# Kernel optimization log

Hardware: AMD Instinct MI355X
Metric: run time of the kernel (lower is better)

The kernel has to match this reference:

```python
import jax, jax.numpy as jnp
import numpy as np

C = 16; HP = 16; WP = 16; D = 32; KITER = 4; P = 8; N = P * P; B = 16; HID = 64


def conv2d(x, w, b):
    # x: (B, Cin, H, W), w: (Cout, Cin, kh, kw), 'same' padding for 3x3
    y = jax.lax.conv_general_dilated(x, w, (1, 1), [(1, 1), (1, 1)],
                                     dimension_numbers=('NCHW', 'OIHW', 'NCHW'))
    return y + b[None, :, None, None]


def setup_inputs() -> dict:
    key = jax.random.key(0)
    ks = jax.random.split(key, 20)
    n = lambda k, shape, s=0.1: jax.random.normal(k, shape, jnp.float32) * s
    # 4-neighbor directed grid edges over P x P nodes
    edges = []
    for p in range(P):
        for q in range(P):
            i = p * P + q
            for dp, dq in ((0, 1), (1, 0), (0, -1), (-1, 0)):
                pp, qq = p + dp, q + dq
                if 0 <= pp < P and 0 <= qq < P:
                    edges.append((i, pp * P + qq))
    edge_index = jnp.asarray(np.asarray(edges, np.int32))  # (E, 2) with (i=dst, j=src)
    return {
        'seed': n(ks[0], (B, C, P * HP, P * WP), 1.0),
        'edge_index': edge_index,
        'wq': n(ks[1], (C, D)), 'bq': jnp.zeros((D,), jnp.float32),
        'wk': n(ks[2], (C, D)), 'bk': jnp.zeros((D,), jnp.float32),
        'wm': n(ks[3], (C, C, 3, 3)), 'bm': jnp.zeros((C,), jnp.float32),
        'a_w1': n(ks[4], (2 * D, HID)), 'a_b1': jnp.zeros((HID,), jnp.float32),
        'a_w2': n(ks[5], (HID, HID)), 'a_b2': jnp.zeros((HID,), jnp.float32),
        'a_wo': n(ks[6], (HID, 1)), 'a_bo': jnp.zeros((1,), jnp.float32),
        'g_w': n(ks[7], (C, 1, 3, 3)), 'g_b': jnp.zeros((C,), jnp.float32),
        'gru_wg': n(ks[8], (2 * C, 2 * C, 3, 3)), 'gru_bg': jnp.zeros((2 * C,), jnp.float32),
        'gru_wc': n(ks[9], (C, 2 * C, 3, 3)), 'gru_bc': jnp.zeros((C,), jnp.float32),
    }


def reference(seed, edge_index, wq, bq, wk, bk, wm, bm,
              a_w1, a_b1, a_w2, a_b2, a_wo, a_bo,
              g_w, g_b, gru_wg, gru_bg, gru_wc, gru_bc):
    Bb, Cc, PH, PW = seed.shape
    Pp = PH // HP
    Nn = Pp * Pp
    # patchify: (B,C,PH,PW) -> (B,N,C,H,W), node order is row-major (p,q)
    X = seed.reshape(Bb, Cc, Pp, HP, Pp, WP).transpose(0, 2, 4, 1, 3, 5).reshape(Bb, Nn, Cc, HP, WP)
    ei = edge_index[:, 0]  # dst node i
    ej = edge_index[:, 1]  # src node j
    # GateConv on a spatially-constant map e: conv(e*ones) = e * conv(ones) (+bias).
    ones_map = jnp.ones((1, 1, HP, WP), seed.dtype)
    T = jax.lax.conv_general_dilated(ones_map, g_w, (1, 1), [(1, 1), (1, 1)],
                                     dimension_numbers=('NCHW', 'OIHW', 'NCHW'))  # (1,C,H,W)
    for _ in range(KITER):
        xm = X.mean((-2, -1))  # (B,N,C); mean commutes with the 1x1 convs f_Q/f_K
        q_vec = xm @ wq + bq   # (B,N,d)
        k_vec = xm @ wk + bk
        M = conv2d(X.reshape(Bb * Nn, Cc, HP, WP), wm, bm).reshape(Bb, Nn, Cc, HP, WP)
        # per-edge attention scores via ConcatMLP
        h0 = jnp.concatenate([q_vec[:, ei], k_vec[:, ej]], axis=-1)  # (B,E,2d)
        h1 = jax.nn.relu(h0 @ a_w1 + a_b1)
        h2 = jax.nn.relu(h1 @ a_w2 + a_b2)
        e = (h2 @ a_wo + a_bo)[..., 0]  # (B,E)
        # gate map and gated messages
        G = jax.nn.sigmoid(e[:, :, None, None, None] * T[None] + g_b[None, None, :, None, None])  # (B,E,C,H,W)
        msg = G * M[:, ej]  # gather src patches, gate
        agg = jax.ops.segment_sum(jnp.moveaxis(msg, 1, 0), ei, num_segments=Nn)  # (N,B,C,H,W)
        M_agg = jnp.moveaxis(agg, 0, 1).reshape(Bb * Nn, Cc, HP, WP)
        # ConvGRU cell update
        h = X.reshape(Bb * Nn, Cc, HP, WP)
        zr = jax.nn.sigmoid(conv2d(jnp.concatenate([M_agg, h], axis=1), gru_wg, gru_bg))
        z, r = zr[:, :Cc], zr[:, Cc:]
        cand = jnp.tanh(conv2d(jnp.concatenate([M_agg, r * h], axis=1), gru_wc, gru_bc))
        X = ((1.0 - z) * h + z * cand).reshape(Bb, Nn, Cc, HP, WP)
    # unpatchify
    out = X.reshape(Bb, Pp, Pp, Cc, HP, WP).transpose(0, 3, 1, 4, 2, 5).reshape(Bb, Cc, PH, PW)
    return out
```

## Files before the change

### kernel.cpp

```cpp
#include <hip/hip_runtime.h>
#include <hip/hip_bf16.h>
#include <hip/hip_cooperative_groups.h>

namespace cg = cooperative_groups;

#define Bt 16
#define Ct 16
#define Nt 64
#define KITERt 4

#define WF_TOTAL 25681
#define SWZ_TOTAL 16384
#define SETUP_IDX (WF_TOTAL + 4096 + Nt + SWZ_TOTAL)
#define SAH_STRIDE 40

typedef __attribute__((ext_vector_type(8))) short bf16x8;
typedef __attribute__((ext_vector_type(4))) short s16x4;
typedef __attribute__((ext_vector_type(4))) float f32x4;

__device__ inline short f2bs(float f) {
    __hip_bfloat16 h = __float2bfloat16(f);
    short s; __builtin_memcpy(&s, &h, 2); return s;
}
__device__ inline float bs2f(short s) {
    __hip_bfloat16 h; __builtin_memcpy(&h, &s, 2);
    return __bfloat162float(h);
}
__device__ inline float loadf(const void* p, int i, int isf32) {
    return isf32 ? ((const float*)p)[i]
                 : __bfloat162float(((const __hip_bfloat16*)p)[i]);
}
__device__ inline float sigm(float x) {
    return __builtin_amdgcn_rcpf(1.f + __expf(-x));
}
__device__ inline float tanh_fast(float x) {
    float e = __expf(2.f * x);
    return 1.f - 2.f * __builtin_amdgcn_rcpf(e + 1.f);
}

__global__ __launch_bounds__(256)
__attribute__((amdgpu_waves_per_eu(4, 4)))
void fused_kernel(
    const void* __restrict__ seed,
    const void* __restrict__ wq, const void* __restrict__ bq,
    const void* __restrict__ wk, const void* __restrict__ bk,
    const void* __restrict__ wm, const void* __restrict__ bm,
    const void* __restrict__ w1, const void* __restrict__ b1,
    const void* __restrict__ w2, const void* __restrict__ b2,
    const void* __restrict__ wo, const void* __restrict__ bo,
    const void* __restrict__ gw, const void* __restrict__ gb,
    const void* __restrict__ wg, const void* __restrict__ bg,
    const void* __restrict__ wc, const void* __restrict__ bc,
    const int* __restrict__ edge, int E,
    float* __restrict__ Wf, float* __restrict__ Tpix,
    int* __restrict__ counts, int* __restrict__ nbrs,
    __hip_bfloat16* __restrict__ swz,
    float* __restrict__ qv0, float* __restrict__ kv0,
    float* __restrict__ qv1, float* __restrict__ kv1,
    float* __restrict__ Mb0, float* __restrict__ Mb1,
    void* __restrict__ out)
{
    __shared__ float sred[4];
    __shared__ int sflag;
    __shared__ float xred[64];
    __shared__ int snb[256];
    __shared__ float evs[4];
    __shared__ __align__(16) short sAH[324 * SAH_STRIDE];
    int bn = blockIdx.x, t = threadIdx.x;
    int b = bn >> 6, i = bn & 63;
    int lane = t & 63, wv = t >> 6;
    int quad = lane >> 4, n16 = lane & 15;
    int pp = ((t >> 4) + 1) * 18 + (t & 15) + 1;

    const short* WgSg = (const short*)swz;
    const short* WcSg = (const short*)(swz + 9216);
    const short* WmSg = (const short*)(swz + 13824);

    {
        float v = fabsf(__bfloat162float(((const __hip_bfloat16*)seed)[t]));
        if (!(v <= 1e30f)) v = 1e30f;
#pragma unroll
        for (int off = 1; off < 64; off <<= 1) v = fmaxf(v, __shfl_xor(v, off, 64));
        if (lane == 0) sred[wv] = v;
        __syncthreads();
        if (t == 0) {
            float m = fmaxf(fmaxf(sred[0], sred[1]), fmaxf(sred[2], sred[3]));
            sflag = (m > 1e10f) ? 1 : 0;
        }
        __syncthreads();
    }
    int isf32 = sflag;

    if (bn == 0) {
        snb[t] = 0;
        __syncthreads();
        for (int e = t; e < E; e += 256) {
            int ei = edge[2 * e], ej = edge[2 * e + 1];
            int d = ej - ei;
            int slot = (d == 1) ? 0 : (d == 8) ? 1 : (d == -1) ? 2 : 3;
            snb[ei * 4 + slot] = ej + 1;
        }
        __syncthreads();
        if (t < 64) {
            int dcount = 0;
            int outv[4] = {0, 0, 0, 0};
#pragma unroll
            for (int s = 0; s < 4; ++s) {
                int v = snb[t * 4 + s];
                if (v) outv[dcount++] = v - 1;
            }
            counts[t] = dcount;
#pragma unroll
            for (int s = 0; s < 4; ++s) nbrs[t * 4 + s] = outv[s];
        }
    }

    int idx = bn * 256 + t;
    if (idx < WF_TOTAL) {
        int ii = idx;
        const void* base;
        if (ii < 512) base = wq;
        else if ((ii -= 512) < 32) base = bq;
        else if ((ii -= 32) < 512) base = wk;
        else if ((ii -= 512) < 32) base = bk;
        else if ((ii -= 32) < 2304) base = wm;
        else if ((ii -= 2304) < 16) base = bm;
        else if ((ii -= 16) < 4096) base = w1;
        else if ((ii -= 4096) < 64) base = b1;
        else if ((ii -= 64) < 4096) base = w2;
        else if ((ii -= 4096) < 64) base = b2;
        else if ((ii -= 64) < 64) base = wo;
        else if ((ii -= 64) < 1) base = bo;
        else if ((ii -= 1) < 16) base = gb;
        else if ((ii -= 16) < 9216) base = wg;
        else if ((ii -= 9216) < 32) base = bg;
        else if ((ii -= 32) < 4608) base = wc;
        else { ii -= 4608; base = bc; }
        Wf[idx] = loadf(base, ii, isf32);
    } else if (idx < WF_TOTAL + 4096) {
        int j = idx - WF_TOTAL;
        int pix = j >> 4, ch = j & 15;
        int y = pix >> 4, x = pix & 15;
        float s = 0.f;
        for (int ky = 0; ky < 3; ++ky)
            for (int kx = 0; kx < 3; ++kx) {
                int yy = y + ky - 1, xx = x + kx - 1;
                if (yy >= 0 && yy < 16 && xx >= 0 && xx < 16)
                    s += loadf(gw, ch * 9 + ky * 3 + kx, isf32);
            }
        Tpix[j] = s;
    } else if (idx >= WF_TOTAL + 4096 + Nt && idx < SETUP_IDX) {
        int j = idx - (WF_TOTAL + 4096 + Nt);
        float val;
        if (j < 9216) {
            int sn = j >> 9, rem = j & 511;
            int ln = rem >> 3, jj = rem & 7;
            int s = sn >> 1, nt = sn & 1;
            int ci = (ln >> 4) * 8 + jj;
            int co = nt * 16 + (ln & 15);
            val = loadf(wg, co * 288 + ci * 9 + s, isf32);
        } else if (j < 9216 + 4608) {
            int j1 = j - 9216;
            int s = j1 >> 9, rem = j1 & 511;
            int ln = rem >> 3, jj = rem & 7;
            int ci = (ln >> 4) * 8 + jj;
            int co = ln & 15;
            val = loadf(wc, co * 288 + ci * 9 + s, isf32);
        } else {
            int j2 = j - 13824;
            int sp = j2 >> 9, rem = j2 & 511;
            int ln = rem >> 3, jj = rem & 7;
            int k = (ln >> 4) * 8 + jj;
            int s = sp * 2 + (k >> 4);
            int ci = k & 15;
            int co = ln & 15;
            val = (s <= 8) ? loadf(wm, co * 144 + ci * 9 + s, isf32) : 0.f;
        }
        swz[j] = __float2bfloat16(val);
    }

    {
        int n = bn & 63;
        int pq = n >> 3, qq = n & 7;
        int y = t >> 4, x = t & 15;
        float v[16];
#pragma unroll
        for (int c = 0; c < 16; ++c)
            v[c] = loadf(seed, ((b * 16 + c) * 128 + pq * 16 + y) * 128 + qq * 16 + x, isf32);
        bf16x8 o0, o1;
#pragma unroll
        for (int c = 0; c < 8; ++c) { o0[c] = f2bs(v[c]); o1[c] = f2bs(v[8 + c]); }

        for (int p = t; p < 324; p += 256) {
            int yy = p / 18 - 1, xx = p % 18 - 1;
            if (!((unsigned)yy < 16u && (unsigned)xx < 16u)) {
                bf16x8 z = {0, 0, 0, 0, 0, 0, 0, 0};
                short* row = sAH + p * SAH_STRIDE;
                *(bf16x8*)(row) = z;      *(bf16x8*)(row + 8) = z;
                *(bf16x8*)(row + 16) = z; *(bf16x8*)(row + 24) = z;
            }
        }
        {
            short* row = sAH + pp * SAH_STRIDE;
            *(bf16x8*)(row) = o0;      *(bf16x8*)(row + 8) = o1;
            *(bf16x8*)(row + 16) = o0; *(bf16x8*)(row + 24) = o1;
        }

#pragma unroll
        for (int c = 0; c < 16; ++c) {
            float s = v[c];
#pragma unroll
            for (int off = 1; off < 64; off <<= 1) s += __shfl_xor(s, off, 64);
            if (lane == c) xred[wv * 16 + c] = s;
        }
        __syncthreads();
        if (t < 64) {
            int d = t & 31;
            float a = (t < 32) ? loadf(bq, d, isf32) : loadf(bk, d, isf32);
#pragma unroll
            for (int c = 0; c < 16; ++c) {
                float xm = (xred[c] + xred[16 + c] + xred[32 + c] + xred[48 + c]) * (1.f / 256.f);
                a += xm * ((t < 32) ? loadf(wq, c * 32 + d, isf32)
                                    : loadf(wk, c * 32 + d, isf32));
            }
            if (t < 32) qv0[bn * 32 + d] = a; else kv0[bn * 32 + d] = a;
        }

        float bm_l = loadf(bm, n16, isf32);
        f32x4 accM[4];
#pragma unroll
        for (int mt = 0; mt < 4; ++mt) accM[mt] = (f32x4){bm_l, bm_l, bm_l, bm_l};
#pragma unroll
        for (int sp = 0; sp < 5; ++sp) {
            int s2 = sp * 2 + (quad >> 1);
            int valid = (s2 <= 8);
            int s2c = valid ? s2 : 8;
            int ky = s2c / 3, kx = s2c - ky * 3;
            bf16x8 Bf;
#pragma unroll
            for (int j = 0; j < 8; ++j) {
                short bv = 0;
                if (valid) bv = f2bs(loadf(wm, n16 * 144 + ((quad & 1) * 8 + j) * 9 + s2, isf32));
                Bf[j] = bv;
            }
            int cib = (quad & 1) * 8;
#pragma unroll
            for (int mt = 0; mt < 4; ++mt) {
                int pc = (wv * 4 + mt + ky) * 18 + n16 + kx;
                bf16x8 A = *(const bf16x8*)(sAH + pc * SAH_STRIDE + cib);
                accM[mt] = __builtin_amdgcn_mfma_f32_16x16x32_bf16(A, Bf, accM[mt], 0, 0, 0);
            }
        }
        float* mo = Mb0 + bn * 4096;
#pragma unroll
        for (int mt = 0; mt < 4; ++mt)
#pragma unroll
            for (int r = 0; r < 4; ++r) {
                int pix = (wv * 4 + mt) * 16 + quad * 4 + r;
                mo[pix * 16 + n16] = accM[mt][r];
            }
    }

    __threadfence();
    cg::this_grid().sync();

    int4 nb4 = *(const int4*)(nbrs + i * 4);
    int deg = counts[i];
    int ejl[4] = {nb4.x, nb4.y, nb4.z, nb4.w};

    for (int it = 0; it < KITERt; ++it) {
        const float* Min  = (it & 1) ? Mb1 : Mb0;
        float*       Mout = (it & 1) ? Mb0 : Mb1;
        const float* qin  = (it & 1) ? qv1 : qv0;
        const float* kin  = (it & 1) ? kv1 : kv0;
        float*       qout = (it & 1) ? qv0 : qv1;
        float*       kout = (it & 1) ? kv0 : kv1;
        int last = (it == KITERt - 1);

        if (wv < deg) {
            int ej = ejl[wv];
            float h0 = (lane < 32) ? qin[bn * 32 + lane]
                                   : kin[(b * 64 + ej) * 32 + (lane - 32)];
            const float* W1 = Wf + 3408;
            const float* W2 = Wf + 7568;
            float p0 = 0.f, p1 = 0.f, p2 = 0.f, p3 = 0.f;
#pragma unroll
            for (int j = 0; j < 64; j += 4) {
                p0 += __shfl(h0, j + 0, 64) * W1[(j + 0) * 64 + lane];
                p1 += __shfl(h0, j + 1, 64) * W1[(j + 1) * 64 + lane];
                p2 += __shfl(h0, j + 2, 64) * W1[(j + 2) * 64 + lane];
                p3 += __shfl(h0, j + 3, 64) * W1[(j + 3) * 64 + lane];
            }
            float a1 = fmaxf(Wf[7504 + lane] + ((p0 + p1) + (p2 + p3)), 0.f);
            p0 = p1 = p2 = p3 = 0.f;
#pragma unroll
            for (int j = 0; j < 64; j += 4) {
                p0 += __shfl(a1, j + 0, 64) * W2[(j + 0) * 64 + lane];
                p1 += __shfl(a1, j + 1, 64) * W2[(j + 1) * 64 + lane];
                p2 += __shfl(a1, j + 2, 64) * W2[(j + 2) * 64 + lane];
                p3 += __shfl(a1, j + 3, 64) * W2[(j + 3) * 64 + lane];
            }
            float a2 = fmaxf(Wf[11664 + lane] + ((p0 + p1) + (p2 + p3)), 0.f);
            float pe = a2 * Wf[11728 + lane];
#pragma unroll
            for (int off = 32; off; off >>= 1) pe += __shfl_down(pe, off, 64);
            if (lane == 0) evs[wv] = pe + Wf[11792];
        }
        __syncthreads();

        float magg[16];
#pragma unroll
        for (int c = 0; c < 16; ++c) magg[c] = 0.f;
        {
            float Tp[16];
#pragma unroll
            for (int c = 0; c < 4; ++c)
                *(f32x4*)(Tp + 4 * c) = *(const f32x4*)(Tpix + t * 16 + 4 * c);
#pragma unroll
            for (int ii = 0; ii < 4; ++ii)
                if (ii < deg) {
                    const float* mp = Min + (b * 64 + ejl[ii]) * 4096 + t * 16;
                    f32x4 m0 = *(const f32x4*)(mp);
                    f32x4 m1 = *(const f32x4*)(mp + 4);
                    f32x4 m2 = *(const f32x4*)(mp + 8);
                    f32x4 m3 = *(const f32x4*)(mp + 12);
                    float evv = evs[ii];
#pragma unroll
                    for (int c = 0; c < 4; ++c) {
                        magg[c]      += sigm(evv * Tp[c]      + Wf[11793 + c])      * m0[c];
                        magg[c + 4]  += sigm(evv * Tp[c + 4]  + Wf[11793 + c + 4])  * m1[c];
                        magg[c + 8]  += sigm(evv * Tp[c + 8]  + Wf[11793 + c + 8])  * m2[c];
                        magg[c + 12] += sigm(evv * Tp[c + 12] + Wf[11793 + c + 12]) * m3[c];
                    }
                }
        }
        {
            bf16x8 mg0, mg1;
#pragma unroll
            for (int c = 0; c < 8; ++c) { mg0[c] = f2bs(magg[c]); mg1[c] = f2bs(magg[c + 8]); }
            *(bf16x8*)(sAH + pp * SAH_STRIDE) = mg0;
            *(bf16x8*)(sAH + pp * SAH_STRIDE + 8) = mg1;
        }
        __syncthreads();

        float bz = Wf[21025 + n16], br = Wf[21025 + 16 + n16];
        f32x4 accZ[4], accR[4];
#pragma unroll
        for (int mt = 0; mt < 4; ++mt) {
            accZ[mt] = (f32x4){bz, bz, bz, bz};
            accR[mt] = (f32x4){br, br, br, br};
        }
#pragma unroll
        for (int s = 0; s < 9; ++s) {
            int ky = s / 3, kx = s - (s / 3) * 3;
            bf16x8 B0 = *(const bf16x8*)(WgSg + (s * 2 + 0) * 512 + lane * 8);
            bf16x8 B1 = *(const bf16x8*)(WgSg + (s * 2 + 1) * 512 + lane * 8);
#pragma unroll
            for (int mt = 0; mt < 4; ++mt) {
                int pc = (wv * 4 + mt + ky) * 18 + n16 + kx;
                bf16x8 A = *(const bf16x8*)(sAH + pc * SAH_STRIDE + quad * 8);
                accZ[mt] = __builtin_amdgcn_mfma_f32_16x16x32_bf16(A, B0, accZ[mt], 0, 0, 0);
                accR[mt] = __builtin_amdgcn_mfma_f32_16x16x32_bf16(A, B1, accR[mt], 0, 0, 0);
            }
        }
        float zf[16], hf[16], rh[16];
#pragma unroll
        for (int mt = 0; mt < 4; ++mt)
#pragma unroll
            for (int r = 0; r < 4; ++r) {
                int k = mt * 4 + r;
                int ps = (wv * 4 + mt + 1) * 18 + quad * 4 + r + 1;
                hf[k] = bs2f(sAH[ps * SAH_STRIDE + 16 + n16]);
                zf[k] = sigm(accZ[mt][r]);
                rh[k] = sigm(accR[mt][r]) * hf[k];
            }
        __syncthreads();
#pragma unroll
        for (int mt = 0; mt < 4; ++mt)
#pragma unroll
            for (int r = 0; r < 4; ++r) {
                int ps = (wv * 4 + mt + 1) * 18 + quad * 4 + r + 1;
                sAH[ps * SAH_STRIDE + 16 + n16] = f2bs(rh[mt * 4 + r]);
            }
        __syncthreads();

        float bcl = Wf[25665 + n16];
        f32x4 accC[4];
#pragma unroll
        for (int mt = 0; mt < 4; ++mt) accC[mt] = (f32x4){bcl, bcl, bcl, bcl};
#pragma unroll
        for (int s = 0; s < 9; ++s) {
            int ky = s / 3, kx = s - (s / 3) * 3;
            bf16x8 Bc = *(const bf16x8*)(WcSg + s * 512 + lane * 8);
#pragma unroll
            for (int mt = 0; mt < 4; ++mt) {
                int pc = (wv * 4 + mt + ky) * 18 + n16 + kx;
                bf16x8 A = *(const bf16x8*)(sAH + pc * SAH_STRIDE + quad * 8);
                accC[mt] = __builtin_amdgcn_mfma_f32_16x16x32_bf16(A, Bc, accC[mt], 0, 0, 0);
            }
        }
        float nxv[16];
#pragma unroll
        for (int mt = 0; mt < 4; ++mt)
#pragma unroll
            for (int r = 0; r < 4; ++r) {
                int k = mt * 4 + r;
                nxv[k] = (1.f - zf[k]) * hf[k] + zf[k] * tanh_fast(accC[mt][r]);
            }

        if (last) {
            int pq = i >> 3, qq = i & 7;
#pragma unroll
            for (int mt = 0; mt < 4; ++mt) {
                long base = ((long)(b * 16 + n16) * 128 + pq * 16 + wv * 4 + mt) * 128
                            + qq * 16 + quad * 4;
                if (isf32) {
                    f32x4 v = {nxv[mt * 4], nxv[mt * 4 + 1], nxv[mt * 4 + 2], nxv[mt * 4 + 3]};
                    *(f32x4*)((float*)out + base) = v;
                } else {
                    s16x4 v = {f2bs(nxv[mt * 4]), f2bs(nxv[mt * 4 + 1]),
                               f2bs(nxv[mt * 4 + 2]), f2bs(nxv[mt * 4 + 3])};
                    *(s16x4*)((short*)out + base) = v;
                }
            }
            return;
        }

        __syncthreads();

        float ssum = 0.f;
#pragma unroll
        for (int mt = 0; mt < 4; ++mt)
#pragma unroll
            for (int r = 0; r < 4; ++r) {
                int k = mt * 4 + r;
                ssum += nxv[k];
                int p = (wv * 4 + mt + 1) * 18 + quad * 4 + r + 1;
                short vb = f2bs(nxv[k]);
                sAH[p * SAH_STRIDE + n16] = vb;
                sAH[p * SAH_STRIDE + 16 + n16] = vb;
            }
        ssum += __shfl_xor(ssum, 16, 64);
        ssum += __shfl_xor(ssum, 32, 64);
        if (lane < 16) xred[wv * 16 + lane] = ssum;
        __syncthreads();

        float bm_l = Wf[3392 + n16];
        f32x4 accM[4];
#pragma unroll
        for (int mt = 0; mt < 4; ++mt) accM[mt] = (f32x4){bm_l, bm_l, bm_l, bm_l};
#pragma unroll
        for (int sp = 0; sp < 5; ++sp) {
            bf16x8 Bf = *(const bf16x8*)(WmSg + sp * 512 + lane * 8);
            int s2 = sp * 2 + (quad >> 1);
            if (s2 > 8) s2 = 8;
            int ky = s2 / 3, kx = s2 - (s2 / 3) * 3;
            int cib = (quad & 1) * 8;
#pragma unroll
            for (int mt = 0; mt < 4; ++mt) {
                int pc = (wv * 4 + mt + ky) * 18 + n16 + kx;
                bf16x8 A = *(const bf16x8*)(sAH + pc * SAH_STRIDE + cib);
                accM[mt] = __builtin_amdgcn_mfma_f32_16x16x32_bf16(A, Bf, accM[mt], 0, 0, 0);
            }
        }
        {
            float* mo = Mout + bn * 4096;
#pragma unroll
            for (int mt = 0; mt < 4; ++mt)
#pragma unroll
                for (int r = 0; r < 4; ++r) {
                    int pix = (wv * 4 + mt) * 16 + quad * 4 + r;
                    mo[pix * 16 + n16] = accM[mt][r];
                }
        }
        if (t < 64) {
            int d = t & 31;
            const float* W = (t < 32) ? Wf : Wf + 544;
            float a = (t < 32) ? Wf[512 + d] : Wf[1056 + d];
#pragma unroll
            for (int c = 0; c < 16; ++c) {
                float xc = (xred[c] + xred[16 + c] + xred[32 + c] + xred[48 + c]) * (1.f / 256.f);
                a += xc * W[c * 32 + d];
            }
            if (t < 32) qout[bn * 32 + d] = a; else kout[bn * 32 + d] = a;
        }
        __threadfence();
        cg::this_grid().sync();
    }
}

__global__ __launch_bounds__(256) void setup_kernel(
    const void* __restrict__ seed,
    const void* __restrict__ wq, const void* __restrict__ bq,
    const void* __restrict__ wk, const void* __restrict__ bk,
    const void* __restrict__ wm, const void* __restrict__ bm,
    const void* __restrict__ w1, const void* __restrict__ b1,
    const void* __restrict__ w2, const void* __restrict__ b2,
    const void* __restrict__ wo, const void* __restrict__ bo,
    const void* __restrict__ gw, const void* __restrict__ gb,
    const void* __restrict__ wg, const void* __restrict__ bg,
    const void* __restrict__ wc, const void* __restrict__ bc,
    const int* __restrict__ edge, int E,
    float* __restrict__ Wf, float* __restrict__ Tpix,
// ... 187 lines not shown
                bf16x8 A = *(const bf16x8*)(sM + pc * SAH_STRIDE + cib);
                accM[mt] = __builtin_amdgcn_mfma_f32_16x16x32_bf16(A, Bf, accM[mt], 0, 0, 0);
            }
        }
        float* mo = M0 + bn * 4096;
#pragma unroll
        for (int mt = 0; mt < 4; ++mt)
#pragma unroll
            for (int r = 0; r < 4; ++r) {
                int pix = (wv * 4 + mt) * 16 + quad * 4 + r;
                mo[pix * 16 + n16] = accM[mt][r];
            }
    }
}

__global__ __launch_bounds__(256, 4) void iter_kernel(
    const short* __restrict__ Xin, short* __restrict__ Xout,
    const float* __restrict__ Min, float* __restrict__ Mout,
    const float* __restrict__ qin, const float* __restrict__ kin,
    float* __restrict__ qout, float* __restrict__ kout,
    const float* __restrict__ Tpix,
    const short* __restrict__ WmS,
    const short* __restrict__ WgS,
    const short* __restrict__ WcS,
    const float* __restrict__ Wf,
    const int* __restrict__ counts, const int* __restrict__ nbrs,
    const int* __restrict__ flagp, void* __restrict__ out, int last)
{
    __shared__ __align__(16) short sAH[324 * SAH_STRIDE];
    __shared__ float evs[4];
// ... 260 lines not shown
    __hip_bfloat16* swz = (__hip_bfloat16*)(ws + 4355600);
    float* Mb0 = ws + 4363792;
    float* Mb1 = ws + 8558096;

    const short* WgS = (const short*)swz;
    const short* WcS = (const short*)(swz + 9216);
    const short* WmS = (const short*)(swz + 13824);

    static int coop_ok = -1;
    if (coop_ok < 0) {
        int dev = 0, ncu = 0, coop = 0;
        hipFuncAttributes attr;
        hipError_t e1 = hipGetDevice(&dev);
        hipDeviceProp_t prop;
        hipError_t e2 = (e1 == hipSuccess) ? hipGetDeviceProperties(&prop, dev) : e1;
        hipError_t e3 = hipFuncGetAttributes(&attr, (const void*)fused_kernel);
        if (e2 == hipSuccess) { ncu = prop.multiProcessorCount; coop = prop.cooperativeLaunch; }
        coop_ok = (e2 == hipSuccess && e3 == hipSuccess && coop &&
                   attr.numRegs > 0 && attr.numRegs <= 128 &&
                   attr.localSizeBytes == 0 &&
                   (long)ncu * 4 >= (long)(Bt * Nt)) ? 1 : 0;
        (void)hipGetLastError();
    }

    if (coop_ok == 1) {
        const void* wq = d_in[2];  const void* bq = d_in[3];
        const void* wk = d_in[4];  const void* bk = d_in[5];
        const void* wm = d_in[6];  const void* bm = d_in[7];
        const void* w1 = d_in[8];  const void* b1 = d_in[9];
        const void* w2 = d_in[10]; const void* b2 = d_in[11];
        const void* wo = d_in[12]; const void* bo = d_in[13];
        const void* gw = d_in[14]; const void* gb = d_in[15];
        const void* wg = d_in[16]; const void* bg = d_in[17];
        const void* wc = d_in[18]; const void* bc = d_in[19];
        void* outp = d_out;

        void* kargs[] = {
            (void*)&seed,
            (void*)&wq, (void*)&bq, (void*)&wk, (void*)&bk,
            (void*)&wm, (void*)&bm, (void*)&w1, (void*)&b1,
            (void*)&w2, (void*)&b2, (void*)&wo, (void*)&bo,
            (void*)&gw, (void*)&gb, (void*)&wg, (void*)&bg,
            (void*)&wc, (void*)&bc,
            (void*)&edge, (void*)&E,
            (void*)&Wf, (void*)&Tpix, (void*)&counts, (void*)&nbrs,
            (void*)&swz,
            (void*)&qv0, (void*)&kv0, (void*)&qv1, (void*)&kv1,
            (void*)&Mb0, (void*)&Mb1, (void*)&outp
        };
        hipError_t rc = hipLaunchCooperativeKernel(
            (const void*)fused_kernel, dim3(Bt * Nt), dim3(256), kargs, 0, stream);
        if (rc == hipSuccess) return;
        (void)hipGetLastError();
        coop_ok = 0;
    }

    setup_kernel<<<Bt * Nt, 256, 0, stream>>>(
        seed,
        d_in[2], d_in[3], d_in[4], d_in[5], d_in[6], d_in[7], d_in[8], d_in[9],
        d_in[10], d_in[11], d_in[12], d_in[13], d_in[14], d_in[15], d_in[16],
        d_in[17], d_in[18], d_in[19],
        edge, E, Wf, Tpix, counts, nbrs, swz, Xb0, qv0, kv0, Mb0, flag);

    short* Xs[2] = {Xb0, Xb1};
    float* Ms[2] = {Mb0, Mb1};
    float* qs[2] = {qv0, qv1};
    float* ks[2] = {kv0, kv1};
    for (int it = 0; it < KITERt; ++it) {
        int in = it & 1, on = in ^ 1;
        int last = (it == KITERt - 1);
        iter_kernel<<<Bt * Nt, 256, 0, stream>>>(
            Xs[in], Xs[on], Ms[in], Ms[on], qs[in], ks[in], qs[on], ks[on],
            Tpix, WmS, WgS, WcS, Wf, counts, nbrs, flag, d_out, last);
    }
}
```

Before: 226.4 us.

## Split fused cooperative kernel into normal setup launch plus cooperative iteration kernel

Replaces the single cooperative kernel that did setup and all iterations with a regular setup_kernel launch followed by a cooperative iter4_kernel that runs the four GRU iterations with grid syncs between them. The setup phase no longer needs the grid-wide barrier and can run at its own occupancy. The iteration kernel reads pre-staged X from global memory instead of rebuilding it. This adds one extra kernel launch and a global round trip for the initial state in exchange for a lighter cooperative kernel.

```diff
diff --git a/kernel.cpp b/kernel.cpp
--- a/kernel.cpp
+++ b/kernel.cpp
@@ -36,457 +36,6 @@
 __device__ inline float tanh_fast(float x) {
     float e = __expf(2.f * x);
     return 1.f - 2.f * __builtin_amdgcn_rcpf(e + 1.f);
-}
-
-__global__ __launch_bounds__(256)
-__attribute__((amdgpu_waves_per_eu(4, 4)))
-void fused_kernel(
-    const void* __restrict__ seed,
-    const void* __restrict__ wq, const void* __restrict__ bq,
-    const void* __restrict__ wk, const void* __restrict__ bk,
-    const void* __restrict__ wm, const void* __restrict__ bm,
-    const void* __restrict__ w1, const void* __restrict__ b1,
-    const void* __restrict__ w2, const void* __restrict__ b2,
-    const void* __restrict__ wo, const void* __restrict__ bo,
-    const void* __restrict__ gw, const void* __restrict__ gb,
-    const void* __restrict__ wg, const void* __restrict__ bg,
-    const void* __restrict__ wc, const void* __restrict__ bc,
-    const int* __restrict__ edge, int E,
-    float* __restrict__ Wf, float* __restrict__ Tpix,
-    int* __restrict__ counts, int* __restrict__ nbrs,
-    __hip_bfloat16* __restrict__ swz,
-    float* __restrict__ qv0, float* __restrict__ kv0,
-    float* __restrict__ qv1, float* __restrict__ kv1,
-    float* __restrict__ Mb0, float* __restrict__ Mb1,
-    void* __restrict__ out)
-{
-    __shared__ float sred[4];
-    __shared__ int sflag;
-    __shared__ float xred[64];
-    __shared__ int snb[256];
-    __shared__ float evs[4];
-    __shared__ __align__(16) short sAH[324 * SAH_STRIDE];
-    int bn = blockIdx.x, t = threadIdx.x;
-    int b = bn >> 6, i = bn & 63;
-    int lane = t & 63, wv = t >> 6;
-    int quad = lane >> 4, n16 = lane & 15;
-    int pp = ((t >> 4) + 1) * 18 + (t & 15) + 1;
-
-    const short* WgSg = (const short*)swz;
-    const short* WcSg = (const short*)(swz + 9216);
-    const short* WmSg = (const short*)(swz + 13824);
-
-    {
-        float v = fabsf(__bfloat162float(((const __hip_bfloat16*)seed)[t]));
-        if (!(v <= 1e30f)) v = 1e30f;
-#pragma unroll
-        for (int off = 1; off < 64; off <<= 1) v = fmaxf(v, __shfl_xor(v, off, 64));
-        if (lane == 0) sred[wv] = v;
-        __syncthreads();
-        if (t == 0) {
-            float m = fmaxf(fmaxf(sred[0], sred[1]), fmaxf(sred[2], sred[3]));
-            sflag = (m > 1e10f) ? 1 : 0;
-        }
-        __syncthreads();
-    }
-    int isf32 = sflag;
-
-    if (bn == 0) {
-        snb[t] = 0;
-        __syncthreads();
-        for (int e = t; e < E; e += 256) {
-            int ei = edge[2 * e], ej = edge[2 * e + 1];
-            int d = ej - ei;
-            int slot = (d == 1) ? 0 : (d == 8) ? 1 : (d == -1) ? 2 : 3;
-            snb[ei * 4 + slot] = ej + 1;
-        }
-        __syncthreads();
-        if (t < 64) {
-            int dcount = 0;
-            int outv[4] = {0, 0, 0, 0};
-#pragma unroll
-            for (int s = 0; s < 4; ++s) {
-                int v = snb[t * 4 + s];
-                if (v) outv[dcount++] = v - 1;
-            }
-            counts[t] = dcount;
-#pragma unroll
-            for (int s = 0; s < 4; ++s) nbrs[t * 4 + s] = outv[s];
-        }
-    }
-
-    int idx = bn * 256 + t;
-    if (idx < WF_TOTAL) {
-        int ii = idx;
-        const void* base;
-        if (ii < 512) base = wq;
-        else if ((ii -= 512) < 32) base = bq;
-        else if ((ii -= 32) < 512) base = wk;
-        else if ((ii -= 512) < 32) base = bk;
-        else if ((ii -= 32) < 2304) base = wm;
-        else if ((ii -= 2304) < 16) base = bm;
-        else if ((ii -= 16) < 4096) base = w1;
-        else if ((ii -= 4096) < 64) base = b1;
-        else if ((ii -= 64) < 4096) base = w2;
-        else if ((ii -= 4096) < 64) base = b2;
-        else if ((ii -= 64) < 64) base = wo;
-        else if ((ii -= 64) < 1) base = bo;
-        else if ((ii -= 1) < 16) base = gb;
-        else if ((ii -= 16) < 9216) base = wg;
-        else if ((ii -= 9216) < 32) base = bg;
-        else if ((ii -= 32) < 4608) base = wc;
-        else { ii -= 4608; base = bc; }
-        Wf[idx] = loadf(base, ii, isf32);
-    } else if (idx < WF_TOTAL + 4096) {
-        int j = idx - WF_TOTAL;
-        int pix = j >> 4, ch = j & 15;
-        int y = pix >> 4, x = pix & 15;
-        float s = 0.f;
-        for (int ky = 0; ky < 3; ++ky)
-            for (int kx = 0; kx < 3; ++kx) {
-                int yy = y + ky - 1, xx = x + kx - 1;
-                if (yy >= 0 && yy < 16 && xx >= 0 && xx < 16)
-                    s += loadf(gw, ch * 9 + ky * 3 + kx, isf32);
-            }
-        Tpix[j] = s;
-    } else if (idx >= WF_TOTAL + 4096 + Nt && idx < SETUP_IDX) {
-        int j = idx - (WF_TOTAL + 4096 + Nt);
-        float val;
-        if (j < 9216) {
-            int sn = j >> 9, rem = j & 511;
-            int ln = rem >> 3, jj = rem & 7;
-            int s = sn >> 1, nt = sn & 1;
-            int ci = (ln >> 4) * 8 + jj;
-            int co = nt * 16 + (ln & 15);
-            val = loadf(wg, co * 288 + ci * 9 + s, isf32);
-        } else if (j < 9216 + 4608) {
-            int j1 = j - 9216;
-            int s = j1 >> 9, rem = j1 & 511;
-            int ln = rem >> 3, jj = rem & 7;
-            int ci = (ln >> 4) * 8 + jj;
-            int co = ln & 15;
-            val = loadf(wc, co * 288 + ci * 9 + s, isf32);
-        } else {
-            int j2 = j - 13824;
-            int sp = j2 >> 9, rem = j2 & 511;
-            int ln = rem >> 3, jj = rem & 7;
-            int k = (ln >> 4) * 8 + jj;
-            int s = sp * 2 + (k >> 4);
-            int ci = k & 15;
-            int co = ln & 15;
-            val = (s <= 8) ? loadf(wm, co * 144 + ci * 9 + s, isf32) : 0.f;
-        }
-        swz[j] = __float2bfloat16(val);
-    }
-
-    {
-        int n = bn & 63;
-        int pq = n >> 3, qq = n & 7;
-        int y = t >> 4, x = t & 15;
-        float v[16];
-#pragma unroll
-        for (int c = 0; c < 16; ++c)
-            v[c] = loadf(seed, ((b * 16 + c) * 128 + pq * 16 + y) * 128 + qq * 16 + x, isf32);
-        bf16x8 o0, o1;
-#pragma unroll
-        for (int c = 0; c < 8; ++c) { o0[c] = f2bs(v[c]); o1[c] = f2bs(v[8 + c]); }
-
-        for (int p = t; p < 324; p += 256) {
-            int yy = p / 18 - 1, xx = p % 18 - 1;
-            if (!((unsigned)yy < 16u && (unsigned)xx < 16u)) {
-                bf16x8 z = {0, 0, 0, 0, 0, 0, 0, 0};
-                short* row = sAH + p * SAH_STRIDE;
-                *(bf16x8*)(row) = z;      *(bf16x8*)(row + 8) = z;
-                *(bf16x8*)(row + 16) = z; *(bf16x8*)(row + 24) = z;
-            }
-        }
-        {
-            short* row = sAH + pp * SAH_STRIDE;
-            *(bf16x8*)(row) = o0;      *(bf16x8*)(row + 8) = o1;
-            *(bf16x8*)(row + 16) = o0; *(bf16x8*)(row + 24) = o1;
-        }
-
-#pragma unroll
-        for (int c = 0; c < 16; ++c) {
-            float s = v[c];
-#pragma unroll
-            for (int off = 1; off < 64; off <<= 1) s += __shfl_xor(s, off, 64);
-            if (lane == c) xred[wv * 16 + c] = s;
-        }
-        __syncthreads();
-        if (t < 64) {
-            int d = t & 31;
-            float a = (t < 32) ? loadf(bq, d, isf32) : loadf(bk, d, isf32);
-#pragma unroll
-            for (int c = 0; c < 16; ++c) {
-                float xm = (xred[c] + xred[16 + c] + xred[32 + c] + xred[48 + c]) * (1.f / 256.f);
-                a += xm * ((t < 32) ? loadf(wq, c * 32 + d, isf32)
-                                    : loadf(wk, c * 32 + d, isf32));
-            }
-            if (t < 32) qv0[bn * 32 + d] = a; else kv0[bn * 32 + d] = a;
-        }
-
-        float bm_l = loadf(bm, n16, isf32);
-        f32x4 accM[4];
-#pragma unroll
-        for (int mt = 0; mt < 4; ++mt) accM[mt] = (f32x4){bm_l, bm_l, bm_l, bm_l};
-#pragma unroll
-        for (int sp = 0; sp < 5; ++sp) {
-            int s2 = sp * 2 + (quad >> 1);
-            int valid = (s2 <= 8);
-            int s2c = valid ? s2 : 8;
-            int ky = s2c / 3, kx = s2c - ky * 3;
-            bf16x8 Bf;
-#pragma unroll
-            for (int j = 0; j < 8; ++j) {
-                short bv = 0;
-                if (valid) bv = f2bs(loadf(wm, n16 * 144 + ((quad & 1) * 8 + j) * 9 + s2, isf32));
-                Bf[j] = bv;
-            }
-            int cib = (quad & 1) * 8;
-#pragma unroll
-            for (int mt = 0; mt < 4; ++mt) {
-                int pc = (wv * 4 + mt + ky) * 18 + n16 + kx;
-                bf16x8 A = *(const bf16x8*)(sAH + pc * SAH_STRIDE + cib);
-                accM[mt] = __builtin_amdgcn_mfma_f32_16x16x32_bf16(A, Bf, accM[mt], 0, 0, 0);
-            }
-        }
-        float* mo = Mb0 + bn * 4096;
-#pragma unroll
-        for (int mt = 0; mt < 4; ++mt)
-#pragma unroll
-            for (int r = 0; r < 4; ++r) {
-                int pix = (wv * 4 + mt) * 16 + quad * 4 + r;
-                mo[pix * 16 + n16] = accM[mt][r];
-            }
-    }
-
-    __threadfence();
-    cg::this_grid().sync();
-
-    int4 nb4 = *(const int4*)(nbrs + i * 4);
-    int deg = counts[i];
-    int ejl[4] = {nb4.x, nb4.y, nb4.z, nb4.w};
-
-    for (int it = 0; it < KITERt; ++it) {
-        const float* Min  = (it & 1) ? Mb1 : Mb0;
-        float*       Mout = (it & 1) ? Mb0 : Mb1;
-        const float* qin  = (it & 1) ? qv1 : qv0;
-        const float* kin  = (it & 1) ? kv1 : kv0;
-        float*       qout = (it & 1) ? qv0 : qv1;
-        float*       kout = (it & 1) ? kv0 : kv1;
-        int last = (it == KITERt - 1);
-
-        if (wv < deg) {
-            int ej = ejl[wv];
-            float h0 = (lane < 32) ? qin[bn * 32 + lane]
-                                   : kin[(b * 64 + ej) * 32 + (lane - 32)];
-            const float* W1 = Wf + 3408;
-            const float* W2 = Wf + 7568;
-            float p0 = 0.f, p1 = 0.f, p2 = 0.f, p3 = 0.f;
-#pragma unroll
-            for (int j = 0; j < 64; j += 4) {
-                p0 += __shfl(h0, j + 0, 64) * W1[(j + 0) * 64 + lane];
-                p1 += __shfl(h0, j + 1, 64) * W1[(j + 1) * 64 + lane];
-                p2 += __shfl(h0, j + 2, 64) * W1[(j + 2) * 64 + lane];
-                p3 += __shfl(h0, j + 3, 64) * W1[(j + 3) * 64 + lane];
-            }
-            float a1 = fmaxf(Wf[7504 + lane] + ((p0 + p1) + (p2 + p3)), 0.f);
-            p0 = p1 = p2 = p3 = 0.f;
-#pragma unroll
-            for (int j = 0; j < 64; j += 4) {
-                p0 += __shfl(a1, j + 0, 64) * W2[(j + 0) * 64 + lane];
-                p1 += __shfl(a1, j + 1, 64) * W2[(j + 1) * 64 + lane];
-                p2 += __shfl(a1, j + 2, 64) * W2[(j + 2) * 64 + lane];
-                p3 += __shfl(a1, j + 3, 64) * W2[(j + 3) * 64 + lane];
-            }
-            float a2 = fmaxf(Wf[11664 + lane] + ((p0 + p1) + (p2 + p3)), 0.f);
-            float pe = a2 * Wf[11728 + lane];
-#pragma unroll
-            for (int off = 32; off; off >>= 1) pe += __shfl_down(pe, off, 64);
-            if (lane == 0) evs[wv] = pe + Wf[11792];
-        }
-        __syncthreads();
-
-        float magg[16];
-#pragma unroll
-        for (int c = 0; c < 16; ++c) magg[c] = 0.f;
-        {
-            float Tp[16];
-#pragma unroll
-            for (int c = 0; c < 4; ++c)
-                *(f32x4*)(Tp + 4 * c) = *(const f32x4*)(Tpix + t * 16 + 4 * c);
-#pragma unroll
-            for (int ii = 0; ii < 4; ++ii)
-                if (ii < deg) {
-                    const float* mp = Min + (b * 64 + ejl[ii]) * 4096 + t * 16;
-                    f32x4 m0 = *(const f32x4*)(mp);
-                    f32x4 m1 = *(const f32x4*)(mp + 4);
-                    f32x4 m2 = *(const f32x4*)(mp + 8);
-                    f32x4 m3 = *(const f32x4*)(mp + 12);
-                    float evv = evs[ii];
-#pragma unroll
-                    for (int c = 0; c < 4; ++c) {
-                        magg[c]      += sigm(evv * Tp[c]      + Wf[11793 + c])      * m0[c];
-                        magg[c + 4]  += sigm(evv * Tp[c + 4]  + Wf[11793 + c + 4])  * m1[c];
-                        magg[c + 8]  += sigm(evv * Tp[c + 8]  + Wf[11793 + c + 8])  * m2[c];
-                        magg[c + 12] += sigm(evv * Tp[c + 12] + Wf[11793 + c + 12]) * m3[c];
-                    }
-                }
-        }
-        {
-            bf16x8 mg0, mg1;
-#pragma unroll
-            for (int c = 0; c < 8; ++c) { mg0[c] = f2bs(magg[c]); mg1[c] = f2bs(magg[c + 8]); }
-            *(bf16x8*)(sAH + pp * SAH_STRIDE) = mg0;
-            *(bf16x8*)(sAH + pp * SAH_STRIDE + 8) = mg1;
-        }
-        __syncthreads();
-
-        float bz = Wf[21025 + n16], br = Wf[21025 + 16 + n16];
-        f32x4 accZ[4], accR[4];
-#pragma unroll
-        for (int mt = 0; mt < 4; ++mt) {
-            accZ[mt] = (f32x4){bz, bz, bz, bz};
-            accR[mt] = (f32x4){br, br, br, br};
-        }
-#pragma unroll
-        for (int s = 0; s < 9; ++s) {
-            int ky = s / 3, kx = s - (s / 3) * 3;
-            bf16x8 B0 = *(const bf16x8*)(WgSg + (s * 2 + 0) * 512 + lane * 8);
-            bf16x8 B1 = *(const bf16x8*)(WgSg + (s * 2 + 1) * 512 + lane * 8);
-#pragma unroll
-            for (int mt = 0; mt < 4; ++mt) {
-                int pc = (wv * 4 + mt + ky) * 18 + n16 + kx;
-                bf16x8 A = *(const bf16x8*)(sAH + pc * SAH_STRIDE + quad * 8);
-                accZ[mt] = __builtin_amdgcn_mfma_f32_16x16x32_bf16(A, B0, accZ[mt], 0, 0, 0);
-                accR[mt] = __builtin_amdgcn_mfma_f32_16x16x32_bf16(A, B1, accR[mt], 0, 0, 0);
-            }
-        }
-        float zf[16], hf[16], rh[16];
-#pragma unroll
-        for (int mt = 0; mt < 4; ++mt)
-#pragma unroll
-            for (int r = 0; r < 4; ++r) {
-                int k = mt * 4 + r;
-                int ps = (wv * 4 + mt + 1) * 18 + quad * 4 + r + 1;
-                hf[k] = bs2f(sAH[ps * SAH_STRIDE + 16 + n16]);
-                zf[k] = sigm(accZ[mt][r]);
-                rh[k] = sigm(accR[mt][r]) * hf[k];
-            }
-        __syncthreads();
-#pragma unroll
-        for (int mt = 0; mt < 4; ++mt)
-#pragma unroll
-            for (int r = 0; r < 4; ++r) {
-                int ps = (wv * 4 + mt + 1) * 18 + quad * 4 + r + 1;
-                sAH[ps * SAH_STRIDE + 16 + n16] = f2bs(rh[mt * 4 + r]);
-            }
-        __syncthreads();
-
-        float bcl = Wf[25665 + n16];
-        f32x4 accC[4];
-#pragma unroll
-        for (int mt = 0; mt < 4; ++mt) accC[mt] = (f32x4){bcl, bcl, bcl, bcl};
-#pragma unroll
-        for (int s = 0; s < 9; ++s) {
-            int ky = s / 3, kx = s - (s / 3) * 3;
-            bf16x8 Bc = *(const bf16x8*)(WcSg + s * 512 + lane * 8);
-#pragma unroll
-            for (int mt = 0; mt < 4; ++mt) {
-                int pc = (wv * 4 + mt + ky) * 18 + n16 + kx;
-                bf16x8 A = *(const bf16x8*)(sAH + pc * SAH_STRIDE + quad * 8);
-                accC[mt] = __builtin_amdgcn_mfma_f32_16x16x32_bf16(A, Bc, accC[mt], 0, 0, 0);
-            }
-        }
-        float nxv[16];
-#pragma unroll
-        for (int mt = 0; mt < 4; ++mt)
-#pragma unroll
-            for (int r = 0; r < 4; ++r) {
-                int k = mt * 4 + r;
-                nxv[k] = (1.f - zf[k]) * hf[k] + zf[k] * tanh_fast(accC[mt][r]);
-            }
-
-        if (last) {
-            int pq = i >> 3, qq = i & 7;
-#pragma unroll
-            for (int mt = 0; mt < 4; ++mt) {
-                long base = ((long)(b * 16 + n16) * 128 + pq * 16 + wv * 4 + mt) * 128
-                            + qq * 16 + quad * 4;
-                if (isf32) {
-                    f32x4 v = {nxv[mt * 4], nxv[mt * 4 + 1], nxv[mt * 4 + 2], nxv[mt * 4 + 3]};
-                    *(f32x4*)((float*)out + base) = v;
-                } else {
-                    s16x4 v = {f2bs(nxv[mt * 4]), f2bs(nxv[mt * 4 + 1]),
-                               f2bs(nxv[mt * 4 + 2]), f2bs(nxv[mt * 4 + 3])};
-                    *(s16x4*)((short*)out + base) = v;
-                }
-            }
-            return;
-        }
-
-        __syncthreads();
-
-        float ssum = 0.f;
-#pragma unroll
-        for (int mt = 0; mt < 4; ++mt)
-#pragma unroll
-            for (int r = 0; r < 4; ++r) {
-                int k = mt * 4 + r;
-                ssum += nxv[k];
-                int p = (wv * 4 + mt + 1) * 18 + quad * 4 + r + 1;
-                short vb = f2bs(nxv[k]);
-                sAH[p * SAH_STRIDE + n16] = vb;
-                sAH[p * SAH_STRIDE + 16 + n16] = vb;
-            }
-        ssum += __shfl_xor(ssum, 16, 64);
-        ssum += __shfl_xor(ssum, 32, 64);
-        if (lane < 16) xred[wv * 16 + lane] = ssum;
-        __syncthreads();
-
-        float bm_l = Wf[3392 + n16];
-        f32x4 accM[4];
-#pragma unroll
-        for (int mt = 0; mt < 4; ++mt) accM[mt] = (f32x4){bm_l, bm_l, bm_l, bm_l};
-#pragma unroll
-        for (int sp = 0; sp < 5; ++sp) {
-            bf16x8 Bf = *(const bf16x8*)(WmSg + sp * 512 + lane * 8);
-            int s2 = sp * 2 + (quad >> 1);
-            if (s2 > 8) s2 = 8;
-            int ky = s2 / 3, kx = s2 - (s2 / 3) * 3;
-            int cib = (quad & 1) * 8;
-#pragma unroll
-            for (int mt = 0; mt < 4; ++mt) {
-                int pc = (wv * 4 + mt + ky) * 18 + n16 + kx;
-                bf16x8 A = *(const bf16x8*)(sAH + pc * SAH_STRIDE + cib);
-                accM[mt] = __builtin_amdgcn_mfma_f32_16x16x32_bf16(A, Bf, accM[mt], 0, 0, 0);
-            }
-        }
-        {
-            float* mo = Mout + bn * 4096;
-#pragma unroll
-            for (int mt = 0; mt < 4; ++mt)
-#pragma unroll
-                for (int r = 0; r < 4; ++r) {
-                    int pix = (wv * 4 + mt) * 16 + quad * 4 + r;
-                    mo[pix * 16 + n16] = accM[mt][r];
-                }
-        }
-        if (t < 64) {
-            int d = t & 31;
-            const float* W = (t < 32) ? Wf : Wf + 544;
-            float a = (t < 32) ? Wf[512 + d] : Wf[1056 + d];
-#pragma unroll
-            for (int c = 0; c < 16; ++c) {
-                float xc = (xred[c] + xred[16 + c] + xred[32 + c] + xred[48 + c]) * (1.f / 256.f);
-                a += xc * W[c * 32 + d];
-            }
-            if (t < 32) qout[bn * 32 + d] = a; else kout[bn * 32 + d] = a;
-        }
-        __threadfence();
-        cg::this_grid().sync();
-    }
 }
 
 __global__ __launch_bounds__(256) void setup_kernel(
@@ -704,6 +253,270 @@
     }
 }
 
+__global__ __launch_bounds__(256)
+__attribute__((amdgpu_waves_per_eu(4, 4)))
+void iter4_kernel(
+    const short* __restrict__ Xin,
+    float* __restrict__ Mb0, float* __restrict__ Mb1,
+    float* __restrict__ qv0, float* __restrict__ kv0,
+    float* __restrict__ qv1, float* __restrict__ kv1,
+    const float* __restrict__ Tpix,
+    const short* __restrict__ WmS,
+    const short* __restrict__ WgS,
+    const short* __restrict__ WcS,
+    const float* __restrict__ Wf,
+    const int* __restrict__ counts, const int* __restrict__ nbrs,
+    const int* __restrict__ flagp, void* __restrict__ out)
+{
+    __shared__ __align__(16) short sAH[324 * SAH_STRIDE];
+    __shared__ float evs[4];
+    __shared__ float xred[64];
+    int bn = blockIdx.x, b = bn >> 6, i = bn & 63;
+    int t = threadIdx.x, lane = t & 63, wv = t >> 6;
+    int quad = lane >> 4, n16 = lane & 15;
+    int pp = ((t >> 4) + 1) * 18 + (t & 15) + 1;
+
+    int4 nb4 = *(const int4*)(nbrs + i * 4);
+    int deg = counts[i];
+    int ejl[4] = {nb4.x, nb4.y, nb4.z, nb4.w};
+
+    const short* xown = Xin + bn * 4096;
+    for (int p = t; p < 324; p += 256) {
+        int yy = p / 18 - 1, xx = p % 18 - 1;
+        short* row = sAH + p * SAH_STRIDE;
+        if ((unsigned)yy < 16u && (unsigned)xx < 16u) {
+            const short* src = xown + (yy * 16 + xx) * 16;
+            *(bf16x8*)(row + 16) = *(const bf16x8*)(src);
+            *(bf16x8*)(row + 24) = *(const bf16x8*)(src + 8);
+        } else {
+            bf16x8 z = {0, 0, 0, 0, 0, 0, 0, 0};
+            *(bf16x8*)(row) = z;      *(bf16x8*)(row + 8) = z;
+            *(bf16x8*)(row + 16) = z; *(bf16x8*)(row + 24) = z;
+        }
+    }
+
+    for (int it = 0; it < KITERt; ++it) {
+        const float* Min  = (it & 1) ? Mb1 : Mb0;
+        float*       Mout = (it & 1) ? Mb0 : Mb1;
+        const float* qin  = (it & 1) ? qv1 : qv0;
+        const float* kin  = (it & 1) ? kv1 : kv0;
+        float*       qout = (it & 1) ? qv0 : qv1;
+        float*       kout = (it & 1) ? kv0 : kv1;
+        int last = (it == KITERt - 1);
+
+        if (wv < deg) {
+            int ej = ejl[wv];
+            float h0 = (lane < 32) ? qin[bn * 32 + lane]
+                                   : kin[(b * 64 + ej) * 32 + (lane - 32)];
+            const float* W1 = Wf + 3408;
+            const float* W2 = Wf + 7568;
+            float p0 = 0.f, p1 = 0.f, p2 = 0.f, p3 = 0.f;
+#pragma unroll
+            for (int j = 0; j < 64; j += 4) {
+                p0 += __shfl(h0, j + 0, 64) * W1[(j + 0) * 64 + lane];
+                p1 += __shfl(h0, j + 1, 64) * W1[(j + 1) * 64 + lane];
+                p2 += __shfl(h0, j + 2, 64) * W1[(j + 2) * 64 + lane];
+                p3 += __shfl(h0, j + 3, 64) * W1[(j + 3) * 64 + lane];
+            }
+            float a1 = fmaxf(Wf[7504 + lane] + ((p0 + p1) + (p2 + p3)), 0.f);
+            p0 = p1 = p2 = p3 = 0.f;
+#pragma unroll
+            for (int j = 0; j < 64; j += 4) {
+                p0 += __shfl(a1, j + 0, 64) * W2[(j + 0) * 64 + lane];
+                p1 += __shfl(a1, j + 1, 64) * W2[(j + 1) * 64 + lane];
+                p2 += __shfl(a1, j + 2, 64) * W2[(j + 2) * 64 + lane];
+                p3 += __shfl(a1, j + 3, 64) * W2[(j + 3) * 64 + lane];
+            }
+            float a2 = fmaxf(Wf[11664 + lane] + ((p0 + p1) + (p2 + p3)), 0.f);
+            float pe = a2 * Wf[11728 + lane];
+#pragma unroll
+            for (int off = 32; off; off >>= 1) pe += __shfl_down(pe, off, 64);
+            if (lane == 0) evs[wv] = pe + Wf[11792];
+        }
+        __syncthreads();
+
+        float magg[16];
+#pragma unroll
+        for (int c = 0; c < 16; ++c) magg[c] = 0.f;
+        {
+            float Tp[16];
+#pragma unroll
+            for (int c = 0; c < 4; ++c)
+                *(f32x4*)(Tp + 4 * c) = *(const f32x4*)(Tpix + t * 16 + 4 * c);
+#pragma unroll
+            for (int ii = 0; ii < 4; ++ii)
+                if (ii < deg) {
+                    const float* mp = Min + (b * 64 + ejl[ii]) * 4096 + t * 16;
+                    f32x4 m0 = *(const f32x4*)(mp);
+                    f32x4 m1 = *(const f32x4*)(mp + 4);
+                    f32x4 m2 = *(const f32x4*)(mp + 8);
+                    f32x4 m3 = *(const f32x4*)(mp + 12);
+                    float evv = evs[ii];
+#pragma unroll
+                    for (int c = 0; c < 4; ++c) {
+                        magg[c]      += sigm(evv * Tp[c]      + Wf[11793 + c])      * m0[c];
+                        magg[c + 4]  += sigm(evv * Tp[c + 4]  + Wf[11793 + c + 4])  * m1[c];
+                        magg[c + 8]  += sigm(evv * Tp[c + 8]  + Wf[11793 + c + 8])  * m2[c];
+                        magg[c + 12] += sigm(evv * Tp[c + 12] + Wf[11793 + c + 12]) * m3[c];
+                    }
+                }
+        }
+        {
+            bf16x8 mg0, mg1;
+#pragma unroll
+            for (int c = 0; c < 8; ++c) { mg0[c] = f2bs(magg[c]); mg1[c] = f2bs(magg[c + 8]); }
+            *(bf16x8*)(sAH + pp * SAH_STRIDE) = mg0;
+            *(bf16x8*)(sAH + pp * SAH_STRIDE + 8) = mg1;
+        }
+        __syncthreads();
+
+        float bz = Wf[21025 + n16], br = Wf[21025 + 16 + n16];
+        f32x4 accZ[4], accR[4];
+#pragma unroll
+        for (int mt = 0; mt < 4; ++mt) {
+            accZ[mt] = (f32x4){bz, bz, bz, bz};
+            accR[mt] = (f32x4){br, br, br, br};
+        }
+#pragma unroll
+        for (int s = 0; s < 9; ++s) {
+            int ky = s / 3, kx = s - (s / 3) * 3;
+            bf16x8 B0 = *(const bf16x8*)(WgS + (s * 2 + 0) * 512 + lane * 8);
+            bf16x8 B1 = *(const bf16x8*)(WgS + (s * 2 + 1) * 512 + lane * 8);
+#pragma unroll
+            for (int mt = 0; mt < 4; ++mt) {
+                int pc = (wv * 4 + mt + ky) * 18 + n16 + kx;
+                bf16x8 A = *(const bf16x8*)(sAH + pc * SAH_STRIDE + quad * 8);
+                accZ[mt] = __builtin_amdgcn_mfma_f32_16x16x32_bf16(A, B0, accZ[mt], 0, 0, 0);
+                accR[mt] = __builtin_amdgcn_mfma_f32_16x16x32_bf16(A, B1, accR[mt], 0, 0, 0);
+            }
+        }
+        float zf[16], hf[16], rh[16];
+#pragma unroll
+        for (int mt = 0; mt < 4; ++mt)
+#pragma unroll
+            for (int r = 0; r < 4; ++r) {
+                int k = mt * 4 + r;
+                int ps = (wv * 4 + mt + 1) * 18 + quad * 4 + r + 1;
+                hf[k] = bs2f(sAH[ps * SAH_STRIDE + 16 + n16]);
+                zf[k] = sigm(accZ[mt][r]);
+                rh[k] = sigm(accR[mt][r]) * hf[k];
+            }
+        __syncthreads();
+#pragma unroll
+        for (int mt = 0; mt < 4; ++mt)
+#pragma unroll
+            for (int r = 0; r < 4; ++r) {
+                int ps = (wv * 4 + mt + 1) * 18 + quad * 4 + r + 1;
+                sAH[ps * SAH_STRIDE + 16 + n16] = f2bs(rh[mt * 4 + r]);
+            }
+        __syncthreads();
+
+        float bcl = Wf[25665 + n16];
+        f32x4 accC[4];
+#pragma unroll
+        for (int mt = 0; mt < 4; ++mt) accC[mt] = (f32x4){bcl, bcl, bcl, bcl};
+#pragma unroll
+        for (int s = 0; s < 9; ++s) {
+            int ky = s / 3, kx = s - (s / 3) * 3;
+            bf16x8 Bc = *(const bf16x8*)(WcS + s * 512 + lane * 8);
+#pragma unroll
+            for (int mt = 0; mt < 4; ++mt) {
+                int pc = (wv * 4 + mt + ky) * 18 + n16 + kx;
+                bf16x8 A = *(const bf16x8*)(sAH + pc * SAH_STRIDE + quad * 8);
+                accC[mt] = __builtin_amdgcn_mfma_f32_16x16x32_bf16(A, Bc, accC[mt], 0, 0, 0);
+            }
+        }
+        float nxv[16];
+#pragma unroll
+        for (int mt = 0; mt < 4; ++mt)
+#pragma unroll
+            for (int r = 0; r < 4; ++r) {
+                int k = mt * 4 + r;
+                nxv[k] = (1.f - zf[k]) * hf[k] + zf[k] * tanh_fast(accC[mt][r]);
+            }
+
+        if (last) {
+            int isf32 = *flagp;
+            int pq = i >> 3, qq = i & 7;
+#pragma unroll
+            for (int mt = 0; mt < 4; ++mt) {
+                long base = ((long)(b * 16 + n16) * 128 + pq * 16 + wv * 4 + mt) * 128
+                            + qq * 16 + quad * 4;
+                if (isf32) {
+                    f32x4 v = {nxv[mt * 4], nxv[mt * 4 + 1], nxv[mt * 4 + 2], nxv[mt * 4 + 3]};
+                    *(f32x4*)((float*)out + base) = v;
+                } else {
+                    s16x4 v = {f2bs(nxv[mt * 4]), f2bs(nxv[mt * 4 + 1]),
+                               f2bs(nxv[mt * 4 + 2]), f2bs(nxv[mt * 4 + 3])};
+                    *(s16x4*)((short*)out + base) = v;
+                }
+            }
+            return;
+        }
+
+        __syncthreads();
+
+        float ssum = 0.f;
+#pragma unroll
+        for (int mt = 0; mt < 4; ++mt)
+#pragma unroll
+            for (int r = 0; r < 4; ++r) {
+                int k = mt * 4 + r;
+                ssum += nxv[k];
+                int p = (wv * 4 + mt + 1) * 18 + quad * 4 + r + 1;
+                short vb = f2bs(nxv[k]);
+                sAH[p * SAH_STRIDE + n16] = vb;
+                sAH[p * SAH_STRIDE + 16 + n16] = vb;
+            }
+        ssum += __shfl_xor(ssum, 16, 64);
+        ssum += __shfl_xor(ssum, 32, 64);
+        if (lane < 16) xred[wv * 16 + lane] = ssum;
+        __syncthreads();
+
+        float bm_l = Wf[3392 + n16];
+        f32x4 accM[4];
+#pragma unroll
+        for (int mt = 0; mt < 4; ++mt) accM[mt] = (f32x4){bm_l, bm_l, bm_l, bm_l};
+#pragma unroll
+        for (int sp = 0; sp < 5; ++sp) {
+            bf16x8 Bf = *(const bf16x8*)(WmS + sp * 512 + lane * 8);
+            int s2 = sp * 2 + (quad >> 1);
+            if (s2 > 8) s2 = 8;
+            int ky = s2 / 3, kx = s2 - (s2 / 3) * 3;
+            int cib = (quad & 1) * 8;
+#pragma unroll
+            for (int mt = 0; mt < 4; ++mt) {
+                int pc = (wv * 4 + mt + ky) * 18 + n16 + kx;
+                bf16x8 A = *(const bf16x8*)(sAH + pc * SAH_STRIDE + cib);
+                accM[mt] = __builtin_amdgcn_mfma_f32_16x16x32_bf16(A, Bf, accM[mt], 0, 0, 0);
+            }
+        }
+        {
+            float* mo = Mout + bn * 4096;
+#pragma unroll
+            for (int mt = 0; mt < 4; ++mt)
+#pragma unroll
+                for (int r = 0; r < 4; ++r) {
+                    int pix = (wv * 4 + mt) * 16 + quad * 4 + r;
+                    mo[pix * 16 + n16] = accM[mt][r];
+                }
+        }
+        if (t < 64) {
+            int d = t & 31;
+            const float* W = (t < 32) ? Wf : Wf + 544;
+            float a = (t < 32) ? Wf[512 + d] : Wf[1056 + d];
+#pragma unroll
+            for (int c = 0; c < 16; ++c) {
+                float xc = (xred[c] + xred[16 + c] + xred[32 + c] + xred[48 + c]) * (1.f / 256.f);
+                a += xc * W[c * 32 + d];
+            }
+            if (t < 32) qout[bn * 32 + d] = a; else kout[bn * 32 + d] = a;
+        }
+        __threadfence();
+        cg::this_grid().sync();
+    }
+}
+
 __global__ __launch_bounds__(256, 4) void iter_kernel(
     const short* __restrict__ Xin, short* __restrict__ Xout,
     const float* __restrict__ Min, float* __restrict__ Mout,
@@ -994,7 +807,7 @@
         hipError_t e1 = hipGetDevice(&dev);
         hipDeviceProp_t prop;
         hipError_t e2 = (e1 == hipSuccess) ? hipGetDeviceProperties(&prop, dev) : e1;
-        hipError_t e3 = hipFuncGetAttributes(&attr, (const void*)fused_kernel);
+        hipError_t e3 = hipFuncGetAttributes(&attr, (const void*)iter4_kernel);
         if (e2 == hipSuccess) { ncu = prop.multiProcessorCount; coop = prop.cooperativeLaunch; }
         coop_ok = (e2 == hipSuccess && e3 == hipSuccess && coop &&
                    attr.numRegs > 0 && attr.numRegs <= 128 &&
@@ -1003,44 +816,29 @@
         (void)hipGetLastError();
     }
 
-    if (coop_ok == 1) {
-        const void* wq = d_in[2];  const void* bq = d_in[3];
-        const void* wk = d_in[4];  const void* bk = d_in[5];
-        const void* wm = d_in[6];  const void* bm = d_in[7];
-        const void* w1 = d_in[8];  const void* b1 = d_in[9];
-        const void* w2 = d_in[10]; const void* b2 = d_in[11];
-        const void* wo = d_in[12]; const void* bo = d_in[13];
-        const void* gw = d_in[14]; const void* gb = d_in[15];
-        const void* wg = d_in[16]; const void* bg = d_in[17];
-        const void* wc = d_in[18]; const void* bc = d_in[19];
-        void* outp = d_out;
-
-        void* kargs[] = {
-            (void*)&seed,
-            (void*)&wq, (void*)&bq, (void*)&wk, (void*)&bk,
-            (void*)&wm, (void*)&bm, (void*)&w1, (void*)&b1,
-            (void*)&w2, (void*)&b2, (void*)&wo, (void*)&bo,
-            (void*)&gw, (void*)&gb, (void*)&wg, (void*)&bg,
-            (void*)&wc, (void*)&bc,
-            (void*)&edge, (void*)&E,
-            (void*)&Wf, (void*)&Tpix, (void*)&counts, (void*)&nbrs,
-            (void*)&swz,
-            (void*)&qv0, (void*)&kv0, (void*)&qv1, (void*)&kv1,
-            (void*)&Mb0, (void*)&Mb1, (void*)&outp
-        };
-        hipError_t rc = hipLaunchCooperativeKernel(
-            (const void*)fused_kernel, dim3(Bt * Nt), dim3(256), kargs, 0, stream);
-        if (rc == hipSuccess) return;
-        (void)hipGetLastError();
-        coop_ok = 0;
-    }
-
     setup_kernel<<<Bt * Nt, 256, 0, stream>>>(
         seed,
         d_in[2], d_in[3], d_in[4], d_in[5], d_in[6], d_in[7], d_in[8], d_in[9],
         d_in[10], d_in[11], d_in[12], d_in[13], d_in[14], d_in[15], d_in[16],
         d_in[17], d_in[18], d_in[19],
         edge, E, Wf, Tpix, counts, nbrs, swz, Xb0, qv0, kv0, Mb0, flag);
+
+    if (coop_ok == 1) {
+        const short* Xin = Xb0;
+        void* outp = d_out;
+        void* kargs[] = {
+            (void*)&Xin,
+            (void*)&Mb0, (void*)&Mb1,
+            (void*)&qv0, (void*)&kv0, (void*)&qv1, (void*)&kv1,
+            (void*)&Tpix, (void*)&WmS, (void*)&WgS, (void*)&WcS, (void*)&Wf,
+            (void*)&counts, (void*)&nbrs, (void*)&flag, (void*)&outp
+        };
+        hipError_t rc = hipLaunchCooperativeKernel(
+            (const void*)iter4_kernel, dim3(Bt * Nt), dim3(256), kargs, 0, stream);
+        if (rc == hipSuccess) return;
+        (void)hipGetLastError();
+        coop_ok = 0;
+    }
 
     short* Xs[2] = {Xb0, Xb1};
     float* Ms[2] = {Mb0, Mb1};
```

Measured after the change: 228.1 us. No clear change (+0.8%).
